# Performance work log

Hardware: AMD Instinct MI355X
Metric: run time of the kernel (lower is better)

Reference implementation:

```python
import jax, jax.numpy as jnp
import numpy as np

N, D_IN = 8192, 1024
FC1, FC2, FC3 = 256, 128, 64
DQK = FC3 // 8  # 8


def setup_inputs() -> dict:
    key = jax.random.key(0)
    ks = jax.random.split(key, 20)
    s = 0.05
    inp = {
        "x": jax.random.normal(ks[0], (N, D_IN), jnp.float32),
        # feature extractor MLP (dropout omitted: eval mode)
        "W1": jax.random.normal(ks[1], (D_IN, FC1), jnp.float32) * s,
        "b1": jnp.zeros((FC1,), jnp.float32),
        "W2": jax.random.normal(ks[2], (FC1, FC2), jnp.float32) * s,
        "b2": jnp.zeros((FC2,), jnp.float32),
        "W3": jax.random.normal(ks[3], (FC2, FC3), jnp.float32) * s,
        "b3": jnp.zeros((FC3,), jnp.float32),
        # 1x1 conv Q/K/V == linear layers on the 64-dim embedding
        "Wq": jax.random.normal(ks[4], (FC3, DQK), jnp.float32) * s,
        "bq": jnp.zeros((DQK,), jnp.float32),
        "Wk": jax.random.normal(ks[5], (FC3, DQK), jnp.float32) * s,
        "bk": jnp.zeros((DQK,), jnp.float32),
        "Wv": jax.random.normal(ks[6], (FC3, FC3), jnp.float32) * s,
        "bv": jnp.zeros((FC3,), jnp.float32),
        "gamma": jnp.array([0.5], jnp.float32),  # learned residual scale (init 0 in torch)
        # attention-pooling branch
        "Wa1": jax.random.normal(ks[7], (FC3, FC3), jnp.float32) * s,
        "ba1": jnp.zeros((FC3,), jnp.float32),
        "Wa2": jax.random.normal(ks[8], (FC3, 1), jnp.float32) * s,
        "ba2": jnp.zeros((1,), jnp.float32),
        # classifier
        "Wc": jax.random.normal(ks[9], (FC3, 1), jnp.float32) * s,
        "bc": jnp.zeros((1,), jnp.float32),
    }
    return inp


def reference(x, W1, b1, W2, b2, W3, b3, Wq, bq, Wk, bk, Wv, bv, gamma,
              Wa1, ba1, Wa2, ba2, Wc, bc):
    # instance feature extractor (dropout identity at eval)
    H = jax.nn.relu(x @ W1 + b1)
    H = jax.nn.relu(H @ W2 + b2)
    H = jax.nn.relu(H @ W3 + b3)                 # [N, 64]
    # self-attention over instances (unscaled dot product)
    Q = H @ Wq + bq                              # [N, 8]
    K = H @ Wk + bk                              # [N, 8]
    V = H @ Wv + bv                              # [N, 64]
    att = jax.nn.softmax(Q @ K.T, axis=-1)       # [N, N] full score matrix
    H = gamma[0] * (att @ V) + H                 # residual scale-add
    # attention-based MIL pooling
    scores = jnp.tanh(H @ Wa1 + ba1) @ Wa2 + ba2 # [N, 1]
    A = jax.nn.softmax(scores[:, 0])             # [N]
    M = A @ H                                    # [64] bag embedding
    Y = jax.nn.sigmoid(M @ Wc + bc)[0]
    Y_prob = jnp.clip(Y, 1e-5, 1.0 - 1e-5)
    return (Y_prob, M)
```

## Files before the change

### kernel.cpp

```cpp
#include <hip/hip_runtime.h>
#include <math.h>

typedef unsigned short ushort_t;
typedef __attribute__((ext_vector_type(8))) short short8;
typedef __attribute__((ext_vector_type(4))) float f32x4;

__device__ inline unsigned bfpair(float lo, float hi) {
  unsigned r;
  asm("v_cvt_pk_bf16_f32 %0, %1, %2" : "=v"(r) : "v"(lo), "v"(hi));
  return r;
}
__device__ inline ushort_t bf16of(float v) { return (ushort_t)(bfpair(v, v) & 0xffffu); }
__device__ inline void permswap32(unsigned &a, unsigned &b) {
  asm("v_permlane32_swap_b32 %0, %1" : "+v"(a), "+v"(b));
}
__device__ inline void permswap16(unsigned &a, unsigned &b) {
  asm("v_permlane16_swap_b32 %0, %1" : "+v"(a), "+v"(b));
}

__device__ void transpose_tile(const float* __restrict__ W, ushort_t* __restrict__ Wt,
                               int K, int N, int bx, int by, int t)
{
  __shared__ float Ls[32][33];
  const int n0 = bx * 32, k0 = by * 32;
  const int tx = t & 31, tyb = t >> 5;
  #pragma unroll
  for (int s = 0; s < 4; ++s) {
    const int k = tyb + s * 8;
    Ls[k][tx] = W[(size_t)(k0 + k) * N + n0 + tx];
  }
  __syncthreads();
  #pragma unroll
  for (int s = 0; s < 2; ++s) {
    const int idx = t + 256 * s;
    const int n = idx >> 4, kk = (idx & 15) * 2;
    const unsigned pk = bfpair(Ls[kk][n], Ls[kk + 1][n]);
    *(unsigned*)&Wt[(size_t)(n0 + n) * K + k0 + kk] = pk;
  }
}

__global__ __launch_bounds__(256) void prep_all_k(
    const float* __restrict__ W1, ushort_t* __restrict__ W1t,
    const float* __restrict__ W2, ushort_t* __restrict__ W2t,
    const float* __restrict__ W3, ushort_t* __restrict__ W3t,
    const float* __restrict__ Wa1, ushort_t* __restrict__ Wa1t,
    const float* __restrict__ Wq, const float* __restrict__ Wk,
    const float* __restrict__ Wv, ushort_t* __restrict__ WqkvT)
{
  const int bid = blockIdx.x;
  const int t = threadIdx.x;
  if (bid < 256)      { transpose_tile(W1, W1t, 1024, 256, bid & 7, bid >> 3, t); }
  else if (bid < 288) { const int l = bid - 256; transpose_tile(W2, W2t, 256, 128, l & 3, l >> 2, t); }
  else if (bid < 296) { const int l = bid - 288; transpose_tile(W3, W3t, 128,  64, l & 1, l >> 1, t); }
  else if (bid < 300) { const int l = bid - 296; transpose_tile(Wa1, Wa1t, 64,  64, l & 1, l >> 1, t); }
  else {
    for (int e = t; e < 80 * 64; e += 256) {
      const int j = e >> 6, k = e & 63;
      float v;
      if (j < 8)       v = Wq[k * 8 + j];
      else if (j < 16) v = Wk[k * 8 + (j - 8)];
      else             v = Wv[k * 64 + (j - 16)];
      WqkvT[e] = bf16of(v);
    }
  }
}

template<int K, int N, int WAVES, bool A_FP32, int OMODE>
__global__ __launch_bounds__(WAVES * 64) void gemm_staged(
    const void* __restrict__ Ap, const ushort_t* __restrict__ Wt,
    const float* __restrict__ bias, void* __restrict__ C0, void* __restrict__ C1)
{
  constexpr int BM = 32;
  constexpr int NWN = N / 32;
  constexpr int NK = K / 32;
  constexpr int A_CH = BM * 4;
  constexpr int B_CH = N * 4;
  static_assert(WAVES * 64 == B_CH, "threads must equal B chunk count");
  static_assert(A_CH <= WAVES * 64, "");

  const int tid = threadIdx.x;
  const int wave = tid >> 6, lane = tid & 63;
  const int ln = lane & 15, g = lane >> 4;
  const int wm = wave / NWN, wn = wave % NWN;
  const int bm0 = blockIdx.x * BM;

  __shared__ ushort_t Als[2][BM][40];
  __shared__ ushort_t Bls[2][N][40];

  const float* Af = (const float*)Ap;
  const ushort_t* Ab = (const ushort_t*)Ap;

  const bool hasA = (tid < A_CH);
  const int arow = tid >> 2, akq = tid & 3;
  const int bc = hasA ? (B_CH - A_CH + tid) : (tid - A_CH);
  const int brow = bc >> 2, bkq = bc & 3;

  float4 rf0, rf1;
  short8 ra, rb;

  auto LOADK = [&](int ks) {
    const int k0 = ks * 32;
    if (hasA) {
      if (A_FP32) {
        const float* src = &Af[(size_t)(bm0 + arow) * K + k0 + akq * 8];
        rf0 = *(const float4*)src;
        rf1 = *(const float4*)(src + 4);
      } else {
        ra = *(const short8*)&Ab[(size_t)(bm0 + arow) * K + k0 + akq * 8];
      }
    }
    rb = *(const short8*)&Wt[(size_t)brow * K + k0 + bkq * 8];
  };
  auto WRITEK = [&](int cur) {
    if (hasA) {
      short8 wa;
      if (A_FP32) {
        union { unsigned u[4]; short8 s8; } cv;
        cv.u[0] = bfpair(rf0.x, rf0.y);
        cv.u[1] = bfpair(rf0.z, rf0.w);
        cv.u[2] = bfpair(rf1.x, rf1.y);
        cv.u[3] = bfpair(rf1.z, rf1.w);
        wa = cv.s8;
      } else {
        wa = ra;
      }
      *(short8*)&Als[cur][arow][akq * 8] = wa;
    }
    *(short8*)&Bls[cur][brow][bkq * 8] = rb;
  };

  f32x4 acc0 = {0.f, 0.f, 0.f, 0.f};
  f32x4 acc1 = {0.f, 0.f, 0.f, 0.f};

  LOADK(0);
  int cur = 0;
  for (int ks = 0; ks < NK; ++ks) {
    WRITEK(cur);
    __syncthreads();
    if (ks + 1 < NK) LOADK(ks + 1);
    const short8 af = *(const short8*)&Als[cur][wm * 16 + ln][g * 8];
    const short8 b0 = *(const short8*)&Bls[cur][wn * 32 + ln][g * 8];
    const short8 b1 = *(const short8*)&Bls[cur][wn * 32 + 16 + ln][g * 8];
    acc0 = __builtin_amdgcn_mfma_f32_16x16x32_bf16(af, b0, acc0, 0, 0, 0);
    acc1 = __builtin_amdgcn_mfma_f32_16x16x32_bf16(af, b1, acc1, 0, 0, 0);
    cur ^= 1;
  }

  #pragma unroll
  for (int nt = 0; nt < 2; ++nt) {
    const f32x4 a = nt ? acc1 : acc0;
    #pragma unroll
    for (int r = 0; r < 4; ++r) {
      const int m = bm0 + wm * 16 + 4 * g + r;
      const int n = wn * 32 + nt * 16 + ln;
      float v = a[r] + bias[n];
      v = fmaxf(v, 0.f);
      if (OMODE == 0) {
        ((ushort_t*)C0)[(size_t)m * N + n] = bf16of(v);
      } else {
        ((float*)C0)[(size_t)m * N + n] = v;
      }
    }
  }
}

__global__ __launch_bounds__(256) void mlp23_qkv_k(
    const ushort_t* __restrict__ H1b, const ushort_t* __restrict__ W2t,
    const float* __restrict__ b2, const ushort_t* __restrict__ W3t,
    const float* __restrict__ b3, const ushort_t* __restrict__ WqkvT,
    const float* __restrict__ bq, const float* __restrict__ bk, const float* __restrict__ bv,
    float* __restrict__ H3, ushort_t* __restrict__ Qb, ushort_t* __restrict__ Kb,
    ushort_t* __restrict__ VT)
{
  const int wave = threadIdx.x >> 6, lane = threadIdx.x & 63;
  const int ln = lane & 15, g = lane >> 4;
  const int q0 = blockIdx.x * 16;
  const f32x4 zero4 = {0.f, 0.f, 0.f, 0.f};

  __shared__ ushort_t H2ls[16][136];
  __shared__ ushort_t Hls[16][72];

  f32x4 a2[2] = {zero4, zero4};
  #pragma unroll 2
  for (int k0 = 0; k0 < 256; k0 += 32) {
    const short8 af = *(const short8*)&H1b[(size_t)(q0 + ln) * 256 + k0 + g * 8];
    const short8 b0 = *(const short8*)&W2t[(size_t)(wave * 32 + ln) * 256 + k0 + g * 8];
    const short8 b1 = *(const short8*)&W2t[(size_t)(wave * 32 + 16 + ln) * 256 + k0 + g * 8];
    a2[0] = __builtin_amdgcn_mfma_f32_16x16x32_bf16(af, b0, a2[0], 0, 0, 0);
    a2[1] = __builtin_amdgcn_mfma_f32_16x16x32_bf16(af, b1, a2[1], 0, 0, 0);
  }
  #pragma unroll
  for (int nt = 0; nt < 2; ++nt)
    #pragma unroll
    for (int r = 0; r < 4; ++r) {
      const int n = wave * 32 + nt * 16 + ln;
      H2ls[4 * g + r][n] = bf16of(fmaxf(a2[nt][r] + b2[n], 0.f));
    }
  __syncthreads();

  f32x4 a3 = zero4;
  #pragma unroll
  for (int k0 = 0; k0 < 128; k0 += 32) {
    const short8 af = *(const short8*)&H2ls[ln][k0 + g * 8];
    const short8 bfr = *(const short8*)&W3t[(size_t)(wave * 16 + ln) * 128 + k0 + g * 8];
    a3 = __builtin_amdgcn_mfma_f32_16x16x32_bf16(af, bfr, a3, 0, 0, 0);
  }
  #pragma unroll
  for (int r = 0; r < 4; ++r) {
    const int m = q0 + 4 * g + r;
    const int n = wave * 16 + ln;
    float v = fmaxf(a3[r] + b3[n], 0.f);
    H3[(size_t)m * 64 + n] = v;
    Hls[4 * g + r][n] = bf16of(v);
  }
  __syncthreads();

  const int ntA = (wave == 0) ? 0 : (wave + 1);
  f32x4 accA = zero4, accB = zero4;
  #pragma unroll
  for (int k0 = 0; k0 < 64; k0 += 32) {
    const short8 af = *(const short8*)&Hls[ln][k0 + g * 8];
    const short8 bA = *(const short8*)&WqkvT[(size_t)(ntA * 16 + ln) * 64 + k0 + g * 8];
    accA = __builtin_amdgcn_mfma_f32_16x16x32_bf16(af, bA, accA, 0, 0, 0);
    if (wave == 0) {
      const short8 bB = *(const short8*)&WqkvT[(size_t)(16 + ln) * 64 + k0 + g * 8];
      accB = __builtin_amdgcn_mfma_f32_16x16x32_bf16(af, bB, accB, 0, 0, 0);
    }
  }
  if (wave == 0) {
    const float b0 = (ln < 8) ? bq[ln] : bk[ln - 8];
    #pragma unroll
    for (int r = 0; r < 4; ++r) {
      const int m = q0 + 4 * g + r;
      const float v = accA[r] + b0;
      if (ln < 8) Qb[(size_t)m * 8 + ln] = bf16of(v);
      else        Kb[(size_t)m * 8 + (ln - 8)] = bf16of(v);
    }
    const int d = ln;
    const float bb = bv[d];
    uint2 o;
    o.x = bfpair(accB[0] + bb, accB[1] + bb);
    o.y = bfpair(accB[2] + bb, accB[3] + bb);
    *(uint2*)&VT[(size_t)d * 8192 + q0 + 4 * g] = o;
  } else {
    const int d = (ntA - 1) * 16 + ln;
    const float bb = bv[d];
    uint2 o;
    o.x = bfpair(accA[0] + bb, accA[1] + bb);
    o.y = bfpair(accA[2] + bb, accA[3] + bb);
    *(uint2*)&VT[(size_t)d * 8192 + q0 + 4 * g] = o;
  }
}

__global__ __launch_bounds__(1024) void attn_part_k(
    const ushort_t* __restrict__ Qb, const ushort_t* __restrict__ Kb,
    const ushort_t* __restrict__ VT, float* __restrict__ Pnum,
    float* __restrict__ Pden)
{
  const int tid = threadIdx.x;
  const int wave = tid >> 6, lane = tid & 63;
  const int m = lane & 15, g = lane >> 4;
  const int qg = blockIdx.x >> 3, js = blockIdx.x & 7;
  const int q0 = qg * 256 + wave * 16;
  const int j0 = js * 1024;
  const f32x4 zero4 = {0.f,0.f,0.f,0.f};

  __shared__ ushort_t Vls[2][64][68];
  __shared__ ushort_t Kls[2][64][12];

  const bool isV = (tid < 512);
  const int vd = tid >> 3, vc = tid & 7;
  const bool isK = (tid >= 512 && tid < 576);
  const int kj = tid - 512;

  short8 vreg = {0,0,0,0,0,0,0,0}, kreg = {0,0,0,0,0,0,0,0};
  auto LOAD = [&](int jb) {
    if (isV) vreg = *(const short8*)&VT[(size_t)vd * 8192 + jb + vc * 8];
    if (isK) kreg = *(const short8*)&Kb[(size_t)(jb + kj) * 8];
  };
  auto WRITE = [&](int cur) {
    if (isV) *(short8*)&Vls[cur][vd][vc * 8] = vreg;
    if (isK) *(short8*)&Kls[cur][kj][0] = kreg;
  };

  short8 qf = {0,0,0,0,0,0,0,0};
  if (lane < 16) qf = *(const short8*)&Qb[(size_t)(q0 + m) * 8];

  f32x4 acc[4];
  #pragma unroll
  for (int dt=0;dt<4;dt++) acc[dt] = zero4;
  float lsum = 0.f;

  LOAD(j0);
  int cur = 0;
  for (int it = 0; it < 16; ++it) {
    WRITE(cur);
    __syncthreads();
    if (it + 1 < 16) LOAD(j0 + (it + 1) * 64);

    #pragma unroll
    for (int half = 0; half < 2; ++half) {
      short8 kf0 = {0,0,0,0,0,0,0,0}, kf1 = {0,0,0,0,0,0,0,0};
      if (lane < 16) {
        kf0 = *(const short8*)&Kls[cur][half*32 + m][0];
        kf1 = *(const short8*)&Kls[cur][half*32 + 16 + m][0];
      }
      const f32x4 s0 = __builtin_amdgcn_mfma_f32_16x16x32_bf16(kf0, qf, zero4, 0,0,0);
      const f32x4 s1 = __builtin_amdgcn_mfma_f32_16x16x32_bf16(kf1, qf, zero4, 0,0,0);
      const float e00 = __expf(s0[0]), e01 = __expf(s0[1]), e02 = __expf(s0[2]), e03 = __expf(s0[3]);
      const float e10 = __expf(s1[0]), e11 = __expf(s1[1]), e12 = __expf(s1[2]), e13 = __expf(s1[3]);
      lsum += ((e00+e01)+(e02+e03)) + ((e10+e11)+(e12+e13));
      unsigned X01 = bfpair(e00,e01), X23 = bfpair(e02,e03);
      unsigned Y01 = bfpair(e10,e11), Y23 = bfpair(e12,e13);
      permswap32(X01, Y01); permswap16(X01, Y01);
      permswap32(X23, Y23); permswap16(X23, Y23);
      union { unsigned u[4]; short8 s; } pfu;
      pfu.u[0] = X01;
      pfu.u[1] = X23;
      pfu.u[2] = Y01;
      pfu.u[3] = Y23;
      #pragma unroll
      for (int dt=0;dt<4;dt++) {
        const short8 vf = *(const short8*)&Vls[cur][dt*16 + m][half*32 + g * 8];
        acc[dt] = __builtin_amdgcn_mfma_f32_16x16x32_bf16(pfu.s, vf, acc[dt], 0,0,0);
      }
    }
    cur ^= 1;
  }

  lsum += __shfl_xor(lsum, 16, 64);
  lsum += __shfl_xor(lsum, 32, 64);

  float* np = &Pnum[((size_t)blockIdx.x * 256 + wave * 16) * 64];
  #pragma unroll
  for (int dt=0;dt<4;dt++)
    #pragma unroll
    for (int r=0;r<4;r++)
      np[(size_t)(4*g + r) * 64 + dt*16 + m] = acc[dt][r];
  if (lane < 16)
    Pden[(size_t)blockIdx.x * 256 + wave * 16 + m] = lsum;
}

__global__ __launch_bounds__(256) void epilogue_k(
    const float* __restrict__ Pnum, const float* __restrict__ Pden,
    const float* __restrict__ H3, const float* __restrict__ gamma,
    const ushort_t* __restrict__ Wa1t, const float* __restrict__ ba1,
    const float* __restrict__ Wa2, const float* __restrict__ ba2,
    float* __restrict__ pM, float* __restrict__ pS)
{
  const int wave = threadIdx.x >> 6, lane = threadIdx.x & 63;
  const int ln = lane & 15, g = lane >> 4;
  const int q0 = blockIdx.x * 64 + wave * 16;
  const f32x4 zero4 = {0.f, 0.f, 0.f, 0.f};

  __shared__ float Hals[4][16][68];
  __shared__ ushort_t Habls[4][16][72];
  __shared__ float scls[4][16];
  __shared__ float Ms[4][64];
  __shared__ float Ss[4];

  const float gm = gamma[0];
  #pragma unroll 4
  for (int r = 0; r < 16; ++r) {
    const int q = q0 + r;
    const int qg = q >> 8, qloc = q & 255;
    float num = 0.f, den = 0.f;
    #pragma unroll
    for (int js = 0; js < 8; ++js) {
      const size_t base = (size_t)(qg * 8 + js) * 256 + qloc;
      num += Pnum[base * 64 + lane];
      den += Pden[base];
    }
    const float hv = fmaf(gm, num / den, H3[(size_t)q * 64 + lane]);
    Hals[wave][r][lane] = hv;
    Habls[wave][r][lane] = bf16of(hv);
  }

  f32x4 acc[4];
  #pragma unroll
  for (int nt = 0; nt < 4; ++nt) acc[nt] = zero4;
  #pragma unroll
  for (int k0 = 0; k0 < 64; k0 += 32) {
    const short8 af = *(const short8*)&Habls[wave][ln][k0 + g * 8];
    #pragma unroll
    for (int nt = 0; nt < 4; ++nt) {
      const short8 bfr = *(const short8*)&Wa1t[(size_t)(nt * 16 + ln) * 64 + k0 + g * 8];
      acc[nt] = __builtin_amdgcn_mfma_f32_16x16x32_bf16(af, bfr, acc[nt], 0, 0, 0);
    }
  }
  #pragma unroll
  for (int r = 0; r < 4; ++r) {
    float s = 0.f;
    #pragma unroll
    for (int nt = 0; nt < 4; ++nt) {
      const int n = nt * 16 + ln;
      s += tanhf(acc[nt][r] + ba1[n]) * Wa2[n];
    }
    s += __shfl_xor(s, 1, 64); s += __shfl_xor(s, 2, 64);
    s += __shfl_xor(s, 4, 64); s += __shfl_xor(s, 8, 64);
    if (ln == 0) scls[wave][4 * g + r] = s + ba2[0];
  }

  float macc = 0.f, se = 0.f;
  #pragma unroll 4
  for (int r = 0; r < 16; ++r) {
    const float e = __expf(scls[wave][r]);
    se += e;
    macc = fmaf(e, Hals[wave][r][lane], macc);
  }
  Ms[wave][lane] = macc;
  if (lane == 0) Ss[wave] = se;
  __syncthreads();
  if (wave == 0) {
    pM[(size_t)blockIdx.x * 64 + lane] = Ms[0][lane] + Ms[1][lane] + Ms[2][lane] + Ms[3][lane];
    if (lane == 0) pS[blockIdx.x] = Ss[0] + Ss[1] + Ss[2] + Ss[3];
  }
}

__global__ void pool2_k(const float* __restrict__ pM, const float* __restrict__ pS,
                        const float* __restrict__ Wc, const float* __restrict__ bc,
                        float* __restrict__ out)
{
  const int lane = threadIdx.x;
  float s_ = pS[lane] + pS[64 + lane];
  s_ += __shfl_xor(s_,1,64);  s_ += __shfl_xor(s_,2,64);
  s_ += __shfl_xor(s_,4,64);  s_ += __shfl_xor(s_,8,64);
  s_ += __shfl_xor(s_,16,64); s_ += __shfl_xor(s_,32,64);
  float m_ = 0.f;
  for (int b = 0; b < 128; ++b) m_ += pM[b * 64 + lane];
  const float Md = m_ / s_;
  out[1 + lane] = Md;
  float yp = Md * Wc[lane];
  yp += __shfl_xor(yp,1,64);  yp += __shfl_xor(yp,2,64);
  yp += __shfl_xor(yp,4,64);  yp += __shfl_xor(yp,8,64);
  yp += __shfl_xor(yp,16,64); yp += __shfl_xor(yp,32,64);
  if (lane == 0) {
    float y = 1.f/(1.f + __expf(-(yp + bc[0])));
    y = fminf(fmaxf(y, 1e-5f), 1.f - 1e-5f);
    out[0] = y;
  }
}

extern "C" void kernel_launch(void* const* d_in, const int* in_sizes, int n_in,
                              void* d_out, int out_size, void* d_ws, size_t ws_size,
                              hipStream_t stream)
{
  const float* x    = (const float*)d_in[0];
  const float* W1   = (const float*)d_in[1];
  const float* b1   = (const float*)d_in[2];
  const float* W2   = (const float*)d_in[3];
  const float* b2   = (const float*)d_in[4];
  const float* W3   = (const float*)d_in[5];
  const float* b3   = (const float*)d_in[6];
  const float* Wq   = (const float*)d_in[7];
  const float* bq   = (const float*)d_in[8];
  const float* Wk   = (const float*)d_in[9];
  const float* bk   = (const float*)d_in[10];
  const float* Wv   = (const float*)d_in[11];
  const float* bv   = (const float*)d_in[12];
  const float* gam  = (const float*)d_in[13];
  const float* Wa1  = (const float*)d_in[14];
  const float* ba1  = (const float*)d_in[15];
  const float* Wa2  = (const float*)d_in[16];
  const float* ba2  = (const float*)d_in[17];
  const float* Wc   = (const float*)d_in[18];
  const float* bc   = (const float*)d_in[19];
  float* out = (float*)d_out;

  char* w = (char*)d_ws;
  float* H3 = (float*)w;        w += (size_t)8192*64*4;
  float* pM = (float*)w;        w += 128*64*4;
  float* pS = (float*)w;        w += 128*4;
  float* Pnum = (float*)w;      w += (size_t)256*256*64*4;
  float* Pden = (float*)w;      w += (size_t)256*256*4;
  ushort_t* H1b = (ushort_t*)w; w += (size_t)8192*256*2;
  ushort_t* Qb  = (ushort_t*)w; w += (size_t)8192*8*2;
  ushort_t* Kb  = (ushort_t*)w; w += (size_t)8192*8*2;
  ushort_t* VT  = (ushort_t*)w; w += (size_t)64*8192*2;
  ushort_t* W1t = (ushort_t*)w; w += (size_t)256*1024*2;
  ushort_t* W2t = (ushort_t*)w; w += (size_t)128*256*2;
  ushort_t* W3t = (ushort_t*)w; w += (size_t)64*128*2;
  ushort_t* Wa1t= (ushort_t*)w; w += (size_t)64*64*2;
  ushort_t* Wqkv= (ushort_t*)w; w += (size_t)80*64*2;

  prep_all_k<<<301, 256, 0, stream>>>(W1, W1t, W2, W2t, W3, W3t, Wa1, Wa1t,
                                      Wq, Wk, Wv, Wqkv);
  gemm_staged<1024,256,16,true ,0><<<256, 1024, 0, stream>>>(x, W1t, b1, H1b, nullptr);
  mlp23_qkv_k<<<512, 256, 0, stream>>>(H1b, W2t, b2, W3t, b3, Wqkv,
                                       bq, bk, bv, H3, Qb, Kb, VT);
  attn_part_k<<<256, 1024, 0, stream>>>(Qb, Kb, VT, Pnum, Pden);
  epilogue_k<<<128, 256, 0, stream>>>(Pnum, Pden, H3, gam, Wa1t, ba1, Wa2, ba2, pM, pS);
  pool2_k<<<1, 64, 0, stream>>>(pM, pS, Wc, bc, out);
}
```

Before: 79.00 us.

## Reorder attention blocks, widen epilogue grid, and parallelize final pooling reduction

The attention-partial kernel now orders its blocks key-chunk-major, so concurrently running blocks read the same K/V slice, which should improve cache reuse. The epilogue is split from 128 to 512 blocks: each block handles 16 query rows, and each wave reduces the partial numerators for 4 of those rows. The MFMA scoring step is repeated identically in every wave, so that work is duplicated in exchange for more parallelism. The final pooling kernel grows from one wave to 16 waves and reduces the now 512 partial sums through shared memory.

```diff
diff --git a/kernel.cpp b/kernel.cpp
--- a/kernel.cpp
+++ b/kernel.cpp
@@ -260,7 +260,7 @@
   const int tid = threadIdx.x;
   const int wave = tid >> 6, lane = tid & 63;
   const int m = lane & 15, g = lane >> 4;
-  const int qg = blockIdx.x >> 3, js = blockIdx.x & 7;
+  const int qg = blockIdx.x & 31, js = blockIdx.x >> 5;
   const int q0 = qg * 256 + wave * 16;
   const int j0 = js * 1024;
   const f32x4 zero4 = {0.f,0.f,0.f,0.f};
@@ -350,38 +350,42 @@
 {
   const int wave = threadIdx.x >> 6, lane = threadIdx.x & 63;
   const int ln = lane & 15, g = lane >> 4;
-  const int q0 = blockIdx.x * 64 + wave * 16;
+  const int e = blockIdx.x;
+  const int sub = e >> 5, qg = e & 31;
+  const int q0 = qg * 256 + sub * 16;
   const f32x4 zero4 = {0.f, 0.f, 0.f, 0.f};
 
-  __shared__ float Hals[4][16][68];
-  __shared__ ushort_t Habls[4][16][72];
-  __shared__ float scls[4][16];
+  __shared__ float Hals[16][68];
+  __shared__ ushort_t Habls[16][72];
+  __shared__ float scls[16];
   __shared__ float Ms[4][64];
   __shared__ float Ss[4];
 
   const float gm = gamma[0];
-  #pragma unroll 4
-  for (int r = 0; r < 16; ++r) {
+  #pragma unroll
+  for (int rr = 0; rr < 4; ++rr) {
+    const int r = wave * 4 + rr;
     const int q = q0 + r;
-    const int qg = q >> 8, qloc = q & 255;
+    const int qloc = q & 255;
     float num = 0.f, den = 0.f;
     #pragma unroll
     for (int js = 0; js < 8; ++js) {
-      const size_t base = (size_t)(qg * 8 + js) * 256 + qloc;
+      const size_t base = (size_t)(js * 32 + qg) * 256 + qloc;
       num += Pnum[base * 64 + lane];
       den += Pden[base];
     }
     const float hv = fmaf(gm, num / den, H3[(size_t)q * 64 + lane]);
-    Hals[wave][r][lane] = hv;
-    Habls[wave][r][lane] = bf16of(hv);
-  }
+    Hals[r][lane] = hv;
+    Habls[r][lane] = bf16of(hv);
+  }
+  __syncthreads();
 
   f32x4 acc[4];
   #pragma unroll
   for (int nt = 0; nt < 4; ++nt) acc[nt] = zero4;
   #pragma unroll
   for (int k0 = 0; k0 < 64; k0 += 32) {
-    const short8 af = *(const short8*)&Habls[wave][ln][k0 + g * 8];
+    const short8 af = *(const short8*)&Habls[ln][k0 + g * 8];
     #pragma unroll
     for (int nt = 0; nt < 4; ++nt) {
       const short8 bfr = *(const short8*)&Wa1t[(size_t)(nt * 16 + ln) * 64 + k0 + g * 8];
@@ -398,46 +402,59 @@
     }
     s += __shfl_xor(s, 1, 64); s += __shfl_xor(s, 2, 64);
     s += __shfl_xor(s, 4, 64); s += __shfl_xor(s, 8, 64);
-    if (ln == 0) scls[wave][4 * g + r] = s + ba2[0];
-  }
-
+    if (ln == 0) scls[4 * g + r] = s + ba2[0];
+  }
   float macc = 0.f, se = 0.f;
-  #pragma unroll 4
-  for (int r = 0; r < 16; ++r) {
-    const float e = __expf(scls[wave][r]);
-    se += e;
-    macc = fmaf(e, Hals[wave][r][lane], macc);
+  #pragma unroll
+  for (int rr = 0; rr < 4; ++rr) {
+    const int r = wave * 4 + rr;
+    const float ee = __expf(scls[r]);
+    se += ee;
+    macc = fmaf(ee, Hals[r][lane], macc);
   }
   Ms[wave][lane] = macc;
   if (lane == 0) Ss[wave] = se;
   __syncthreads();
   if (wave == 0) {
-    pM[(size_t)blockIdx.x * 64 + lane] = Ms[0][lane] + Ms[1][lane] + Ms[2][lane] + Ms[3][lane];
-    if (lane == 0) pS[blockIdx.x] = Ss[0] + Ss[1] + Ss[2] + Ss[3];
-  }
-}
-
-__global__ void pool2_k(const float* __restrict__ pM, const float* __restrict__ pS,
-                        const float* __restrict__ Wc, const float* __restrict__ bc,
-                        float* __restrict__ out)
-{
-  const int lane = threadIdx.x;
-  float s_ = pS[lane] + pS[64 + lane];
-  s_ += __shfl_xor(s_,1,64);  s_ += __shfl_xor(s_,2,64);
-  s_ += __shfl_xor(s_,4,64);  s_ += __shfl_xor(s_,8,64);
-  s_ += __shfl_xor(s_,16,64); s_ += __shfl_xor(s_,32,64);
+    pM[(size_t)e * 64 + lane] = Ms[0][lane] + Ms[1][lane] + Ms[2][lane] + Ms[3][lane];
+    if (lane == 0) pS[e] = Ss[0] + Ss[1] + Ss[2] + Ss[3];
+  }
+}
+
+__global__ __launch_bounds__(1024) void pool2_k(
+    const float* __restrict__ pM, const float* __restrict__ pS,
+    const float* __restrict__ Wc, const float* __restrict__ bc,
+    float* __restrict__ out)
+{
+  const int wave = threadIdx.x >> 6, lane = threadIdx.x & 63;
+  __shared__ float Ms2[16][64];
+  __shared__ float Ss2[16];
   float m_ = 0.f;
-  for (int b = 0; b < 128; ++b) m_ += pM[b * 64 + lane];
-  const float Md = m_ / s_;
-  out[1 + lane] = Md;
-  float yp = Md * Wc[lane];
-  yp += __shfl_xor(yp,1,64);  yp += __shfl_xor(yp,2,64);
-  yp += __shfl_xor(yp,4,64);  yp += __shfl_xor(yp,8,64);
-  yp += __shfl_xor(yp,16,64); yp += __shfl_xor(yp,32,64);
-  if (lane == 0) {
-    float y = 1.f/(1.f + __expf(-(yp + bc[0])));
-    y = fminf(fmaxf(y, 1e-5f), 1.f - 1e-5f);
-    out[0] = y;
+  #pragma unroll
+  for (int i = 0; i < 32; ++i)
+    m_ += pM[(size_t)(wave * 32 + i) * 64 + lane];
+  Ms2[wave][lane] = m_;
+  float s_ = (lane < 32) ? pS[wave * 32 + lane] : 0.f;
+  s_ += __shfl_xor(s_, 1, 64);  s_ += __shfl_xor(s_, 2, 64);
+  s_ += __shfl_xor(s_, 4, 64);  s_ += __shfl_xor(s_, 8, 64);
+  s_ += __shfl_xor(s_, 16, 64); s_ += __shfl_xor(s_, 32, 64);
+  if (lane == 0) Ss2[wave] = s_;
+  __syncthreads();
+  if (wave == 0) {
+    float mm = 0.f, ss = 0.f;
+    #pragma unroll
+    for (int i = 0; i < 16; ++i) { mm += Ms2[i][lane]; ss += Ss2[i]; }
+    const float Md = mm / ss;
+    out[1 + lane] = Md;
+    float yp = Md * Wc[lane];
+    yp += __shfl_xor(yp, 1, 64);  yp += __shfl_xor(yp, 2, 64);
+    yp += __shfl_xor(yp, 4, 64);  yp += __shfl_xor(yp, 8, 64);
+    yp += __shfl_xor(yp, 16, 64); yp += __shfl_xor(yp, 32, 64);
+    if (lane == 0) {
+      float y = 1.f / (1.f + __expf(-(yp + bc[0])));
+      y = fminf(fmaxf(y, 1e-5f), 1.f - 1e-5f);
+      out[0] = y;
+    }
   }
 }
 
@@ -469,8 +486,8 @@
 
   char* w = (char*)d_ws;
   float* H3 = (float*)w;        w += (size_t)8192*64*4;
-  float* pM = (float*)w;        w += 128*64*4;
-  float* pS = (float*)w;        w += 128*4;
+  float* pM = (float*)w;        w += 512*64*4;
+  float* pS = (float*)w;        w += 512*4;
   float* Pnum = (float*)w;      w += (size_t)256*256*64*4;
   float* Pden = (float*)w;      w += (size_t)256*256*4;
   ushort_t* H1b = (ushort_t*)w; w += (size_t)8192*256*2;
@@ -489,6 +506,6 @@
   mlp23_qkv_k<<<512, 256, 0, stream>>>(H1b, W2t, b2, W3t, b3, Wqkv,
                                        bq, bk, bv, H3, Qb, Kb, VT);
   attn_part_k<<<256, 1024, 0, stream>>>(Qb, Kb, VT, Pnum, Pden);
-  epilogue_k<<<128, 256, 0, stream>>>(Pnum, Pden, H3, gam, Wa1t, ba1, Wa2, ba2, pM, pS);
-  pool2_k<<<1, 64, 0, stream>>>(pM, pS, Wc, bc, out);
-}
+  epilogue_k<<<512, 256, 0, stream>>>(Pnum, Pden, H3, gam, Wa1t, ba1, Wa2, ba2, pM, pS);
+  pool2_k<<<1, 1024, 0, stream>>>(pM, pS, Wc, bc, out);
+}
```

Result: no change. 77.80 us (-1.5%).
